# Optimization experiments

Hardware: AMD Instinct MI355X
Metric: run time of the kernel (lower is better)

## Reference

```python
import jax, jax.numpy as jnp
import numpy as np

HEADS = 12
IDX = 0


def setup_inputs() -> dict:
    key = jax.random.key(0)
    ks = jax.random.split(key, 6)
    B, H, W, C = 16, 64, 64, 384
    x = jax.random.normal(ks[0], (B, H * W, C), dtype=jnp.float32)
    qkv_w = jax.random.normal(ks[1], (3 * C, C), dtype=jnp.float32) * 0.02
    proj_w = jax.random.normal(ks[2], (C, C), dtype=jnp.float32) * 0.02
    proj_b = jax.random.normal(ks[3], (C,), dtype=jnp.float32) * 0.02
    lepe_w = jax.random.normal(ks[4], (C, 1, 3, 3), dtype=jnp.float32) * 0.02  # depthwise, torch OIHW with I=1
    lepe_b = jax.random.normal(ks[5], (C,), dtype=jnp.float32) * 0.02
    return {"x": x, "qkv_w": qkv_w, "proj_w": proj_w, "proj_b": proj_b,
            "lepe_w": lepe_w, "lepe_b": lepe_b, "H": H, "W": W}


def _lepe_forward(x, qkv_w, proj_w, proj_b, lepe_w, lepe_b, H, W):
    B, N, C = x.shape
    hd = C // HEADS
    scale = hd ** (-0.5)
    x_img = x.reshape(B, H, W, C)

    if IDX == 0:
        # vertical strips: attend over H within each column
        x_split = jnp.transpose(x_img, (0, 2, 1, 3)).reshape(B * W, H, C)
    else:
        x_split = x_img.reshape(B * H, W, C)
    S, L, _ = x_split.shape

    qkv = (x_split @ qkv_w.T).reshape(S, L, 3, HEADS, hd)
    qkv = jnp.transpose(qkv, (2, 0, 3, 1, 4))  # (3, S, heads, L, hd)
    q, k, v = qkv[0], qkv[1], qkv[2]

    attn = jnp.einsum('shld,shmd->shlm', q, k) * scale
    attn = jax.nn.softmax(attn, axis=-1)
    out = jnp.einsum('shlm,shmd->shld', attn, v)           # (S, heads, L, hd)
    out = jnp.transpose(out, (0, 2, 1, 3)).reshape(S, L, C)
    # faithful to torch: view(B, out_H, out_W, C).view(B, H*W, C) -- no permute back for idx==0
    out_flat = out.reshape(B, H * W, C)

    # depthwise 3x3 conv LePE on the original (H, W) layout
    lepe = jax.lax.conv_general_dilated(
        jnp.transpose(x_img, (0, 3, 1, 2)), lepe_w,
        window_strides=(1, 1), padding='SAME',
        feature_group_count=C,
        dimension_numbers=('NCHW', 'OIHW', 'NCHW'))
    lepe = lepe + lepe_b[None, :, None, None]
    lepe = jnp.transpose(lepe, (0, 2, 3, 1)).reshape(B, H * W, C)

    return (out_flat + lepe) @ proj_w.T + proj_b


def reference(x, qkv_w, proj_w, proj_b, lepe_w, lepe_b, H, W):
    return _lepe_forward(x, qkv_w, proj_w, proj_b, lepe_w, lepe_b, H, W)
```

## Files before the change

kernel.cpp:

```cpp
#include <hip/hip_runtime.h>


typedef _Float16 f16;
typedef _Float16 f16x8 __attribute__((ext_vector_type(8)));
typedef float    f32x4 __attribute__((ext_vector_type(4)));

__device__ __forceinline__ f32x4 mfma_16x16x32(f16x8 a, f16x8 b, f32x4 c) {
  return __builtin_amdgcn_mfma_f32_16x16x32_f16(a, b, c, 0, 0, 0);
}

__device__ __forceinline__ void gl_lds16(const f16* g, f16* l) {
  __builtin_amdgcn_global_load_lds((const __attribute__((address_space(1))) void*)g,
                                   (__attribute__((address_space(3))) void*)l, 16, 0, 0);
}

__global__ __launch_bounds__(256) void k_cvt(const float* __restrict__ src,
                                             f16* __restrict__ dst, int n8) {
  int i = blockIdx.x * 256 + threadIdx.x;
  if (i >= n8) return;
  const f32x4* s4 = (const f32x4*)src;
  f32x4 a = s4[2 * i], b = s4[2 * i + 1];
  f16x8 o;
#pragma unroll
  for (int j = 0; j < 4; ++j) { o[j] = (f16)a[j]; o[4 + j] = (f16)b[j]; }
  *(f16x8*)&dst[(long)i * 8] = o;
}

__global__ __launch_bounds__(256) void k_prep(const float* __restrict__ x,
                                              const float* __restrict__ lw,
                                              const float* __restrict__ lb,
                                              f16* __restrict__ x16,
                                              f16* __restrict__ lepe16) {
  __shared__ float ws[9 * 384];
  __shared__ float bs[384];
  for (int i = threadIdx.x; i < 3456; i += 256) {
    int c = i / 9, tap = i - c * 9;
    ws[tap * 384 + (c & 7) * 48 + (c >> 3)] = lw[i];
  }
  for (int i = threadIdx.x; i < 384; i += 256)
    bs[(i & 7) * 48 + (i >> 3)] = lb[i];
  __syncthreads();

  int chunk = blockIdx.x * 256 + threadIdx.x;
  int token = chunk / 48;
  int c0 = (chunk - token * 48) * 8;
  int cg = c0 >> 3;
  int b = token >> 12, n = token & 4095, h = n >> 6, w = n & 63;
  const float* xb = x + (long)(b << 12) * 384;

  float a8[8];
#pragma unroll
  for (int cc = 0; cc < 8; ++cc) a8[cc] = bs[cc * 48 + cg];
  f16x8 cv;
#pragma unroll
  for (int ky = 0; ky < 3; ++ky) {
    int hh = h + ky - 1;
    if (hh < 0 || hh > 63) continue;
#pragma unroll
    for (int kx = 0; kx < 3; ++kx) {
      int ww = w + kx - 1;
      if (ww < 0 || ww > 63) continue;
      const float* p = xb + (long)((hh << 6) + ww) * 384 + c0;
      float4 u = *(const float4*)p;
      float4 v = *(const float4*)(p + 4);
      float xs[8] = {u.x, u.y, u.z, u.w, v.x, v.y, v.z, v.w};
      if (ky == 1 && kx == 1) {
#pragma unroll
        for (int cc = 0; cc < 8; ++cc) cv[cc] = (f16)xs[cc];
      }
      int tap = ky * 3 + kx;
#pragma unroll
      for (int cc = 0; cc < 8; ++cc)
        a8[cc] += xs[cc] * ws[tap * 384 + cc * 48 + cg];
    }
  }
  f16x8 o;
#pragma unroll
  for (int cc = 0; cc < 8; ++cc) o[cc] = (f16)a8[cc];
  *(f16x8*)&x16[(long)token * 384 + c0] = cv;
  *(f16x8*)&lepe16[(long)token * 384 + c0] = o;
}

__global__ __launch_bounds__(512) void k_qkv(const f16* __restrict__ A,
                                             const f16* __restrict__ Bt,
                                             f16* __restrict__ C) {
  __shared__ alignas(16) f16 smem[49152];
  f16* ebuf = smem;
  const int tid = threadIdx.x;
  const int lane = tid & 63;
  const int wave = tid >> 6;
  const int wr = wave >> 1, wc = wave & 1;
  const int ln = lane & 15, quad = lane >> 4;
  const int bid = blockIdx.x;
  const int xcd = bid & 7;
  const int s = bid >> 3;
  const int mq = s / 9;
  const int mt = xcd * 32 + mq;
  const int nt = s - mq * 9;
  const long m0 = (long)mt * 256;
  const int n0 = nt * 128;

  auto stage = [&](int buf, int k0) {
    f16* Asb = smem + buf * 16384;
    f16* Bsb = smem + 32768 + buf * 8192;
#pragma unroll
    for (int r = 0; r < 4; ++r) {
      int flat = r * 512 + tid;
      int row = flat >> 3, c8 = flat & 7;
      int sc8 = (c8 ^ (row & 7)) * 8;
      gl_lds16(&A[(m0 + row) * 384 + k0 + sc8], &Asb[flat * 8]);
    }
#pragma unroll
    for (int r = 0; r < 2; ++r) {
      int flat = r * 512 + tid;
      int row = flat >> 3, c8 = flat & 7;
      int sc8 = (c8 ^ (row & 7)) * 8;
      gl_lds16(&Bt[(long)(n0 + row) * 384 + k0 + sc8], &Bsb[flat * 8]);
    }
  };

  f32x4 acc[4][4] = {};
  stage(0, 0);
  __syncthreads();
  int cur = 0;
  for (int t = 0; t < 6; ++t) {
    if (t < 5) stage(cur ^ 1, (t + 1) * 64);
    const f16* Ac = smem + cur * 16384;
    const f16* Bc = smem + 32768 + cur * 8192;
#pragma unroll
    for (int ks = 0; ks < 2; ++ks) {
      f16x8 a[4], b[4];
#pragma unroll
      for (int i = 0; i < 4; ++i)
        a[i] = *(const f16x8*)&Ac[(wr * 64 + i * 16 + ln) * 64 +
                                  ((ks * 4 + quad) ^ (ln & 7)) * 8];
#pragma unroll
      for (int j = 0; j < 4; ++j)
        b[j] = *(const f16x8*)&Bc[(wc * 64 + j * 16 + ln) * 64 +
                                  ((ks * 4 + quad) ^ (ln & 7)) * 8];
#pragma unroll
      for (int i = 0; i < 4; ++i)
#pragma unroll
        for (int j = 0; j < 4; ++j)
          acc[i][j] = mfma_16x16x32(a[i], b[j], acc[i][j]);
    }
    __syncthreads();
    cur ^= 1;
  }

  for (int p = 0; p < 2; ++p) {
    if ((wr >> 1) == p) {
      const int lr0 = (wr & 1) * 64;
#pragma unroll
      for (int i = 0; i < 4; ++i)
#pragma unroll
        for (int j = 0; j < 4; ++j)
#pragma unroll
          for (int r = 0; r < 4; ++r)
            ebuf[(lr0 + i * 16 + quad * 4 + r) * 136 + wc * 64 + j * 16 + ln] =
                (f16)acc[i][j][r];
    }
    __syncthreads();
#pragma unroll
    for (int it = 0; it < 4; ++it) {
      int flat = it * 512 + tid;
      int row = flat >> 4;
      int c8 = flat & 15;
      int t = (int)m0 + p * 128 + row;
      int nn = t & 4095;
      long prow = (long)(t & ~4095) + ((nn & 63) << 6) + (nn >> 6);
      *(f16x8*)&C[prow * 1152 + n0 + c8 * 8] =
          *(const f16x8*)&ebuf[row * 136 + c8 * 8];
    }
    __syncthreads();
  }
}

__global__ __launch_bounds__(256) void k_attn(const f16* __restrict__ qkv,
                                              f16* __restrict__ attnout) {
  __shared__ alignas(16) f16 shp[4][7424];
  const int lane = threadIdx.x & 63;
  const int wave = threadIdx.x >> 6;
  const int ln = lane & 15, quad = lane >> 4, q8 = quad * 8;
  const int b = blockIdx.x >> 6, w = blockIdx.x & 63;
  const long sbase = (long)b * 4096 + (long)w * 64;

  f16* qs = shp[wave];
  f16* ks = shp[wave] + 2560;
  f16* vt = shp[wave] + 5120;
  f16* ps = shp[wave];
  f16* obuf = shp[wave];
  const float qscale = 0.17677669529663687f;

  for (int hi = 0; hi < 3; ++hi) {
    const int hh = wave * 3 + hi;
#pragma unroll
    for (int r = 0; r < 4; ++r) {
      int flat = r * 64 + lane;
      int l = flat >> 2, dg = (flat & 3) * 8;
      long ta = (sbase + l) * 1152 + hh * 32 + dg;
      f16x8 qv = *(const f16x8*)&qkv[ta];
      f16x8 kv = *(const f16x8*)&qkv[ta + 384];
      f16x8 vv = *(const f16x8*)&qkv[ta + 768];
#pragma unroll
      for (int ii = 0; ii < 8; ++ii) qv[ii] = (f16)((float)qv[ii] * qscale);
      *(f16x8*)&qs[l * 40 + dg] = qv;
      *(f16x8*)&ks[l * 40 + dg] = kv;
#pragma unroll
      for (int ii = 0; ii < 8; ++ii) vt[(dg + ii) * 72 + l] = vv[ii];
    }
    f16x8 aq[4], bk[4];
#pragma unroll
    for (int i = 0; i < 4; ++i) aq[i] = *(const f16x8*)&qs[(i * 16 + ln) * 40 + q8];
#pragma unroll
    for (int j = 0; j < 4; ++j) bk[j] = *(const f16x8*)&ks[(j * 16 + ln) * 40 + q8];
    f32x4 sc[4][4] = {};
#pragma unroll
    for (int i = 0; i < 4; ++i)
#pragma unroll
      for (int j = 0; j < 4; ++j) sc[i][j] = mfma_16x16x32(aq[i], bk[j], sc[i][j]);

    float rs[4][4];
#pragma unroll
    for (int i = 0; i < 4; ++i)
#pragma unroll
      for (int r = 0; r < 4; ++r) {
        float m = -1e30f;
#pragma unroll
        for (int j = 0; j < 4; ++j) m = fmaxf(m, sc[i][j][r]);
#pragma unroll
        for (int off = 1; off < 16; off <<= 1) m = fmaxf(m, __shfl_xor(m, off, 64));
        float sum = 0.f;
#pragma unroll
        for (int j = 0; j < 4; ++j) {
          float p = __expf(sc[i][j][r] - m);
          sc[i][j][r] = p;
          sum += p;
        }
#pragma unroll
        for (int off = 1; off < 16; off <<= 1) sum += __shfl_xor(sum, off, 64);
        rs[i][r] = 1.0f / sum;
      }

#pragma unroll
    for (int i = 0; i < 4; ++i)
#pragma unroll
      for (int j = 0; j < 4; ++j)
#pragma unroll
        for (int r = 0; r < 4; ++r)
          ps[(i * 16 + quad * 4 + r) * 72 + j * 16 + ln] = (f16)sc[i][j][r];

    f32x4 oc[4][2] = {};
#pragma unroll
    for (int k2 = 0; k2 < 2; ++k2) {
      f16x8 ap[4], bv[2];
#pragma unroll
      for (int i = 0; i < 4; ++i)
        ap[i] = *(const f16x8*)&ps[(i * 16 + ln) * 72 + k2 * 32 + q8];
#pragma unroll
      for (int j = 0; j < 2; ++j)
        bv[j] = *(const f16x8*)&vt[(j * 16 + ln) * 72 + k2 * 32 + q8];
#pragma unroll
      for (int i = 0; i < 4; ++i)
#pragma unroll
        for (int j = 0; j < 2; ++j) oc[i][j] = mfma_16x16x32(ap[i], bv[j], oc[i][j]);
    }

#pragma unroll
    for (int i = 0; i < 4; ++i)
#pragma unroll
      for (int j = 0; j < 2; ++j)
#pragma unroll
        for (int r = 0; r < 4; ++r)
          obuf[(i * 16 + quad * 4 + r) * 40 + j * 16 + ln] =
              (f16)(oc[i][j][r] * rs[i][r]);
    {
      int row = lane >> 1, hf = lane & 1;
#pragma unroll
      for (int rr = 0; rr < 2; ++rr) {
        int rw = rr * 32 + row;
        const f16* ob = &obuf[rw * 40 + hf * 16];
        f16x8 o0 = *(const f16x8*)ob;
        f16x8 o1 = *(const f16x8*)(ob + 8);
        f16* gp = attnout + (sbase + rw) * 384 + hh * 32 + hf * 16;
        *(f16x8*)gp = o0;
        *(f16x8*)(gp + 8) = o1;
      }
    }
  }
}

__global__ __launch_bounds__(256) void k_proj(const f16* __restrict__ A1,
                                              const f16* __restrict__ A2,
                                              const f16* __restrict__ Bt,
                                              const float* __restrict__ bias,
                                              float* __restrict__ Cf) {
  __shared__ alignas(16) f16 smem[2 * 128 * 64];
  f16* As = smem;
  f16* Bs = smem + 128 * 64;
  float* buff = (float*)smem;
  const int tid = threadIdx.x;
  const int lane = tid & 63;
  const int wave = tid >> 6;
  const int wr = wave >> 1, wc = wave & 1;
  const int ln = lane & 15, quad = lane >> 4;
  const int bid = blockIdx.x;
  const int xcd = bid & 7;
  const int s = bid >> 3;
  const int mq = s / 3;
  const int mt = xcd * 64 + mq;
  const int nt = s - mq * 3;
  const long m0 = (long)mt * 128;
  const int n0 = nt * 128;

  f32x4 acc[4][4] = {};
  for (int k0 = 0; k0 < 384; k0 += 64) {
#pragma unroll
    for (int r = 0; r < 4; ++r) {
      int flat = r * 256 + tid;
      int row = flat >> 3, c8 = flat & 7;
      int sc8 = (c8 ^ (row & 7)) * 8;
      long ai = (m0 + row) * 384 + k0 + sc8;
      f16x8 s2 = *(const f16x8*)&A1[ai] + *(const f16x8*)&A2[ai];
      *(f16x8*)&As[flat * 8] = s2;
      gl_lds16(&Bt[(long)(n0 + row) * 384 + k0 + sc8], &Bs[flat * 8]);
    }
    __syncthreads();
#pragma unroll
    for (int ks = 0; ks < 2; ++ks) {
      f16x8 a[4], b[4];
#pragma unroll
      for (int i = 0; i < 4; ++i)
        a[i] = *(const f16x8*)&As[(wr * 64 + i * 16 + ln) * 64 +
                                  ((ks * 4 + quad) ^ (ln & 7)) * 8];
#pragma unroll
      for (int j = 0; j < 4; ++j)
        b[j] = *(const f16x8*)&Bs[(wc * 64 + j * 16 + ln) * 64 +
                                  ((ks * 4 + quad) ^ (ln & 7)) * 8];
#pragma unroll
      for (int i = 0; i < 4; ++i)
#pragma unroll
        for (int j = 0; j < 4; ++j)
          acc[i][j] = mfma_16x16x32(a[i], b[j], acc[i][j]);
    }
    __syncthreads();
  }

#pragma unroll
  for (int p = 0; p < 4; ++p) {
    __syncthreads();
    if (wr == (p >> 1)) {
      const int ib = (p & 1) * 2;
#pragma unroll
      for (int ii = 0; ii < 2; ++ii)
#pragma unroll
        for (int j = 0; j < 4; ++j)
#pragma unroll
          for (int r = 0; r < 4; ++r)
            buff[(ii * 16 + quad * 4 + r) * 132 + wc * 64 + j * 16 + ln] =
                acc[ib + ii][j][r];
    }
    __syncthreads();
#pragma unroll
    for (int it = 0; it < 4; ++it) {
      int flat = it * 256 + tid;
      int row = flat >> 5;
      int c4 = flat & 31;
      long gr = m0 + p * 32 + row;
      int col = n0 + c4 * 4;
      float4 b4 = *(const float4*)&bias[col];
      float4 o = *(const float4*)&buff[row * 132 + c4 * 4];
      o.x += b4.x; o.y += b4.y; o.z += b4.z; o.w += b4.w;
      *(float4*)&Cf[gr * 384 + col] = o;
    }
  }
}

extern "C" void kernel_launch(void* const* d_in, const int* in_sizes, int n_in,
                              void* d_out, int out_size, void* d_ws, size_t ws_size,
                              hipStream_t stream) {
  const float* x = (const float*)d_in[0];
  const float* qkv_w = (const float*)d_in[1];
  const float* proj_w = (const float*)d_in[2];
  const float* proj_b = (const float*)d_in[3];
  const float* lepe_w = (const float*)d_in[4];
  const float* lepe_b = (const float*)d_in[5];
  float* out = (float*)d_out;

  char* ws = (char*)d_ws;
  f16* w16 = (f16*)(ws + 0);
  f16* pw16 = (f16*)(ws + 884736);
  f16* x16 = (f16*)(ws + 1179648);
  f16* attnout = x16;
  f16* lepe16 = (f16*)(ws + 51511296);
  f16* qkv16 = (f16*)(ws + 101842944);

  k_cvt<<<216, 256, 0, stream>>>(qkv_w, w16, 55296);
  k_cvt<<<72, 256, 0, stream>>>(proj_w, pw16, 18432);
  k_prep<<<12288, 256, 0, stream>>>(x, lepe_w, lepe_b, x16, lepe16);
  k_qkv<<<2304, 512, 0, stream>>>(x16, w16, qkv16);
  k_attn<<<1024, 256, 0, stream>>>(qkv16, attnout);
  k_proj<<<512 * 3, 256, 0, stream>>>(attnout, lepe16, pw16, proj_b, out);
}
```

Baseline: 456.9 us.

## Fuse attention and output projection into one kernel, keeping outputs in registers

Merges the attention kernel and the projection GEMM. Per-head attention outputs stay in registers as packed f16 pairs, are staged head by head through a double-buffered LDS chunk, get the LePE term added, and are multiplied by the projection weights read directly from global memory. This removes the attnout write and read round trip and one kernel launch. In exchange it adds register pressure (launch bounds of 2 blocks), uncached global loads of the weight B fragments, and a barrier per K chunk.

```diff
diff --git a/kernel.cpp b/kernel.cpp
--- a/kernel.cpp
+++ b/kernel.cpp
@@ -2,6 +2,7 @@
 
 
 typedef _Float16 f16;
+typedef _Float16 f16x2 __attribute__((ext_vector_type(2)));
 typedef _Float16 f16x8 __attribute__((ext_vector_type(8)));
 typedef float    f32x4 __attribute__((ext_vector_type(4)));
 
@@ -176,9 +177,13 @@
   }
 }
 
-__global__ __launch_bounds__(256) void k_attn(const f16* __restrict__ qkv,
-                                              f16* __restrict__ attnout) {
+__global__ __launch_bounds__(256, 2) void k_attnproj(const f16* __restrict__ qkv,
+                                                     const f16* __restrict__ lepe16,
+                                                     const f16* __restrict__ pw,
+                                                     const float* __restrict__ bias,
+                                                     float* __restrict__ outf) {
   __shared__ alignas(16) f16 shp[4][7424];
+  __shared__ alignas(16) f16 aschunk[2][64 * 40];
   const int lane = threadIdx.x & 63;
   const int wave = threadIdx.x >> 6;
   const int ln = lane & 15, quad = lane >> 4, q8 = quad * 8;
@@ -189,8 +194,9 @@
   f16* ks = shp[wave] + 2560;
   f16* vt = shp[wave] + 5120;
   f16* ps = shp[wave];
-  f16* obuf = shp[wave];
   const float qscale = 0.17677669529663687f;
+
+  f16x2 ph0[16], ph1[16], ph2[16];
 
   for (int hi = 0; hi < 3; ++hi) {
     const int hh = wave * 3 + hi;
@@ -269,109 +275,83 @@
 #pragma unroll
     for (int i = 0; i < 4; ++i)
 #pragma unroll
-      for (int j = 0; j < 2; ++j)
+      for (int r = 0; r < 4; ++r) {
+        f16x2 pk;
+        pk[0] = (f16)(oc[i][0][r] * rs[i][r]);
+        pk[1] = (f16)(oc[i][1][r] * rs[i][r]);
+        if (hi == 0) ph0[i * 4 + r] = pk;
+        else if (hi == 1) ph1[i * 4 + r] = pk;
+        else ph2[i * 4 + r] = pk;
+      }
+  }
+
+#define WRITECHUNK(BI, PH)                                        \
+  {                                                               \
+    _Pragma("unroll") for (int i = 0; i < 4; ++i)                 \
+        _Pragma("unroll") for (int r = 0; r < 4; ++r) {           \
+      int row = i * 16 + quad * 4 + r;                            \
+      aschunk[BI][row * 40 + ln] = PH[i * 4 + r][0];              \
+      aschunk[BI][row * 40 + 16 + ln] = PH[i * 4 + r][1];         \
+    }                                                             \
+  }
+
+  if (wave == 0) WRITECHUNK(0, ph0);
+  __syncthreads();
+
+  f32x4 pacc[4][6] = {};
+  const int ncol0 = wave * 96;
+#pragma unroll
+  for (int c = 0; c < 12; ++c) {
+    if (c + 1 < 12 && (c + 1) / 3 == wave) {
+      const int h = (c + 1) % 3;
+      if (h == 0) WRITECHUNK((c + 1) & 1, ph0)
+      else if (h == 1) WRITECHUNK((c + 1) & 1, ph1)
+      else WRITECHUNK((c + 1) & 1, ph2)
+    }
+    const f16* ac = aschunk[c & 1];
+    f16x8 afr[4], bfr[6];
+#pragma unroll
+    for (int i = 0; i < 4; ++i) {
+      f16x8 av = *(const f16x8*)&ac[(i * 16 + ln) * 40 + q8];
+      f16x8 lv = *(const f16x8*)&lepe16[(sbase + i * 16 + ln) * 384 + c * 32 + q8];
+      afr[i] = av + lv;
+    }
+#pragma unroll
+    for (int j = 0; j < 6; ++j)
+      bfr[j] = *(const f16x8*)&pw[(long)(ncol0 + j * 16 + ln) * 384 + c * 32 + q8];
+#pragma unroll
+    for (int i = 0; i < 4; ++i)
+#pragma unroll
+      for (int j = 0; j < 6; ++j)
+        pacc[i][j] = mfma_16x16x32(afr[i], bfr[j], pacc[i][j]);
+    __syncthreads();
+  }
+#undef WRITECHUNK
+
+  float* ebuf = (float*)&shp[0][0];
+#pragma unroll
+  for (int p = 0; p < 2; ++p) {
+    __syncthreads();
+#pragma unroll
+    for (int ii = 0; ii < 2; ++ii)
+#pragma unroll
+      for (int j = 0; j < 6; ++j)
 #pragma unroll
         for (int r = 0; r < 4; ++r)
-          obuf[(i * 16 + quad * 4 + r) * 40 + j * 16 + ln] =
-              (f16)(oc[i][j][r] * rs[i][r]);
-    {
-      int row = lane >> 1, hf = lane & 1;
-#pragma unroll
-      for (int rr = 0; rr < 2; ++rr) {
-        int rw = rr * 32 + row;
-        const f16* ob = &obuf[rw * 40 + hf * 16];
-        f16x8 o0 = *(const f16x8*)ob;
-        f16x8 o1 = *(const f16x8*)(ob + 8);
-        f16* gp = attnout + (sbase + rw) * 384 + hh * 32 + hf * 16;
-        *(f16x8*)gp = o0;
-        *(f16x8*)(gp + 8) = o1;
-      }
-    }
-  }
-}
-
-__global__ __launch_bounds__(256) void k_proj(const f16* __restrict__ A1,
-                                              const f16* __restrict__ A2,
-                                              const f16* __restrict__ Bt,
-                                              const float* __restrict__ bias,
-                                              float* __restrict__ Cf) {
-  __shared__ alignas(16) f16 smem[2 * 128 * 64];
-  f16* As = smem;
-  f16* Bs = smem + 128 * 64;
-  float* buff = (float*)smem;
-  const int tid = threadIdx.x;
-  const int lane = tid & 63;
-  const int wave = tid >> 6;
-  const int wr = wave >> 1, wc = wave & 1;
-  const int ln = lane & 15, quad = lane >> 4;
-  const int bid = blockIdx.x;
-  const int xcd = bid & 7;
-  const int s = bid >> 3;
-  const int mq = s / 3;
-  const int mt = xcd * 64 + mq;
-  const int nt = s - mq * 3;
-  const long m0 = (long)mt * 128;
-  const int n0 = nt * 128;
-
-  f32x4 acc[4][4] = {};
-  for (int k0 = 0; k0 < 384; k0 += 64) {
-#pragma unroll
-    for (int r = 0; r < 4; ++r) {
-      int flat = r * 256 + tid;
-      int row = flat >> 3, c8 = flat & 7;
-      int sc8 = (c8 ^ (row & 7)) * 8;
-      long ai = (m0 + row) * 384 + k0 + sc8;
-      f16x8 s2 = *(const f16x8*)&A1[ai] + *(const f16x8*)&A2[ai];
-      *(f16x8*)&As[flat * 8] = s2;
-      gl_lds16(&Bt[(long)(n0 + row) * 384 + k0 + sc8], &Bs[flat * 8]);
-    }
-    __syncthreads();
-#pragma unroll
-    for (int ks = 0; ks < 2; ++ks) {
-      f16x8 a[4], b[4];
-#pragma unroll
-      for (int i = 0; i < 4; ++i)
-        a[i] = *(const f16x8*)&As[(wr * 64 + i * 16 + ln) * 64 +
-                                  ((ks * 4 + quad) ^ (ln & 7)) * 8];
-#pragma unroll
-      for (int j = 0; j < 4; ++j)
-        b[j] = *(const f16x8*)&Bs[(wc * 64 + j * 16 + ln) * 64 +
-                                  ((ks * 4 + quad) ^ (ln & 7)) * 8];
-#pragma unroll
-      for (int i = 0; i < 4; ++i)
-#pragma unroll
-        for (int j = 0; j < 4; ++j)
-          acc[i][j] = mfma_16x16x32(a[i], b[j], acc[i][j]);
-    }
-    __syncthreads();
-  }
-
-#pragma unroll
-  for (int p = 0; p < 4; ++p) {
-    __syncthreads();
-    if (wr == (p >> 1)) {
-      const int ib = (p & 1) * 2;
-#pragma unroll
-      for (int ii = 0; ii < 2; ++ii)
-#pragma unroll
-        for (int j = 0; j < 4; ++j)
-#pragma unroll
-          for (int r = 0; r < 4; ++r)
-            buff[(ii * 16 + quad * 4 + r) * 132 + wc * 64 + j * 16 + ln] =
-                acc[ib + ii][j][r];
-    }
-    __syncthreads();
-#pragma unroll
-    for (int it = 0; it < 4; ++it) {
-      int flat = it * 256 + tid;
-      int row = flat >> 5;
-      int c4 = flat & 31;
-      long gr = m0 + p * 32 + row;
-      int col = n0 + c4 * 4;
+          ebuf[(ii * 16 + quad * 4 + r) * 388 + ncol0 + j * 16 + ln] =
+              pacc[p * 2 + ii][j][r];
+    __syncthreads();
+#pragma unroll
+    for (int it = 0; it < 12; ++it) {
+      int flat = it * 256 + threadIdx.x;
+      int row = flat / 96;
+      int c4 = flat - row * 96;
+      long gr = sbase + p * 32 + row;
+      int col = c4 * 4;
       float4 b4 = *(const float4*)&bias[col];
-      float4 o = *(const float4*)&buff[row * 132 + c4 * 4];
+      float4 o = *(const float4*)&ebuf[row * 388 + col];
       o.x += b4.x; o.y += b4.y; o.z += b4.z; o.w += b4.w;
-      *(float4*)&Cf[gr * 384 + col] = o;
+      *(float4*)&outf[gr * 384 + col] = o;
     }
   }
 }
@@ -391,7 +371,6 @@
   f16* w16 = (f16*)(ws + 0);
   f16* pw16 = (f16*)(ws + 884736);
   f16* x16 = (f16*)(ws + 1179648);
-  f16* attnout = x16;
   f16* lepe16 = (f16*)(ws + 51511296);
   f16* qkv16 = (f16*)(ws + 101842944);
 
@@ -399,6 +378,5 @@
   k_cvt<<<72, 256, 0, stream>>>(proj_w, pw16, 18432);
   k_prep<<<12288, 256, 0, stream>>>(x, lepe_w, lepe_b, x16, lepe16);
   k_qkv<<<2304, 512, 0, stream>>>(x16, w16, qkv16);
-  k_attn<<<1024, 256, 0, stream>>>(qkv16, attnout);
-  k_proj<<<512 * 3, 256, 0, stream>>>(attnout, lepe16, pw16, proj_b, out);
-}
+  k_attnproj<<<1024, 256, 0, stream>>>(qkv16, lepe16, pw16, proj_b, out);
+}
```

Result: no change. 461.1 us (+0.9%).
